# Kernel tuning notes

Hardware: AMD Instinct MI355X
Metric: run time of the kernel (lower is better)

## Reference

```python
import jax, jax.numpy as jnp
import numpy as np

B, L, D = 1, 1024, 128
EPS = 1e-5


def setup_inputs() -> dict:
    key = jax.random.key(0)
    ks = jax.random.split(key, 10)
    s = 1.0 / np.sqrt(D)
    return {
        "x": jax.random.normal(ks[0], (B, L, D), dtype=jnp.float32),
        "mask": jax.random.randint(ks[1], (B, L, L), 0, 2, dtype=jnp.int32),
        # JCrossOutProduct.l : Linear(D, D)
        "Wl": jax.random.uniform(ks[2], (D, D), jnp.float32, -s, s),
        "bl": jax.random.uniform(ks[3], (D,), jnp.float32, -s, s),
        # JCrossOutProduct.lo : Linear(D, D)
        "Wlo": jax.random.uniform(ks[4], (D, D), jnp.float32, -s, s),
        "blo": jax.random.uniform(ks[5], (D,), jnp.float32, -s, s),
        # JResCOPAttn.l : Linear(D, D)
        "Wl2": jax.random.uniform(ks[6], (D, D), jnp.float32, -s, s),
        "bl2": jax.random.uniform(ks[7], (D,), jnp.float32, -s, s),
        # LayerNorm(D)
        "gamma": jnp.ones((D,), jnp.float32),
        "beta": jnp.zeros((D,), jnp.float32),
    }


def reference(x, mask, Wl, bl, Wlo, blo, Wl2, bl2, gamma, beta):
    # a = self.cop.l(x) : [B, L, D]
    a = x @ Wl.T + bl
    # outer product kept per-channel: [B, L, L, D]
    outer = jnp.einsum('blc,bmc->blmc', a, a)
    # self.cop.lo over last dim: [B, L, L, D]
    tm = outer @ Wlo.T + blo
    # masked_fill(mask.unsqueeze(-1) == 0, 0.0)
    tm = tm * (mask[..., None] != 0).astype(tm.dtype)
    # tx = self.l(x)
    tx = x @ Wl2.T + bl2
    # per-channel attention-like contraction: out[b,c,d] = sum_a tm[b,c,a,d] * tx[b,a,d]
    y = x + jnp.einsum('bcad,bad->bcd', tm, tx)
    # shadow (eval): Dropout=identity, activator 'none'=identity, LayerNorm(D)
    mu = jnp.mean(y, axis=-1, keepdims=True)
    var = jnp.mean(jnp.square(y - mu), axis=-1, keepdims=True)
    return (y - mu) * jax.lax.rsqrt(var + EPS) * gamma + beta
```

## Files before the change

kernel.cpp:

```cpp
#include <hip/hip_runtime.h>
#include <hip/hip_fp16.h>


typedef _Float16 f16x8 __attribute__((ext_vector_type(8)));
typedef float    f32x4 __attribute__((ext_vector_type(4)));

#define LL   1024
#define DD   128
#define EPSV 1e-5f

__global__ __launch_bounds__(256) void prep_kernel(
    const float* __restrict__ x,  const float* __restrict__ Wl,
    const float* __restrict__ bl, const float* __restrict__ Wlo,
    const float* __restrict__ Wl2,const float* __restrict__ bl2,
    _Float16* __restrict__ a_h, float* __restrict__ tx_out,
    _Float16* __restrict__ wh)
{
    __shared__ float xs[16*128];
    __shared__ float wsh[64*129];
    const int t  = threadIdx.x;
    const int bx = blockIdx.x;
    const int by = blockIdx.y;
    const int l0 = by*16;

    #pragma unroll
    for (int i = 0; i < 8; ++i) { int f = i*256 + t; xs[f] = x[l0*DD + f]; }
    const float* Wsrc = ((bx < 2) ? Wl : Wl2) + (bx & 1)*64*DD;
    #pragma unroll
    for (int i = 0; i < 32; ++i) {
        int f = i*256 + t; int r = f >> 7, k = f & 127;
        wsh[r*129 + k] = Wsrc[f];
    }
    __syncthreads();

    const int col  = t & 63;
    const int lsub = t >> 6;
    const float4* X4 = (const float4*)xs;
    float acc0 = 0.f, acc1 = 0.f, acc2 = 0.f, acc3 = 0.f;
    #pragma unroll
    for (int k4 = 0; k4 < 32; ++k4) {
        const float* wp = wsh + col*129 + k4*4;
        float4 wv = {wp[0], wp[1], wp[2], wp[3]};
        float4 x0 = X4[(lsub*4+0)*32 + k4];
        float4 x1 = X4[(lsub*4+1)*32 + k4];
        float4 x2 = X4[(lsub*4+2)*32 + k4];
        float4 x3 = X4[(lsub*4+3)*32 + k4];
        acc0 += wv.x*x0.x + wv.y*x0.y + wv.z*x0.z + wv.w*x0.w;
        acc1 += wv.x*x1.x + wv.y*x1.y + wv.z*x1.z + wv.w*x1.w;
        acc2 += wv.x*x2.x + wv.y*x2.y + wv.z*x2.z + wv.w*x2.w;
        acc3 += wv.x*x3.x + wv.y*x3.y + wv.z*x3.z + wv.w*x3.w;
    }
    const int colg = (bx & 1)*64 + col;
    const float bv = ((bx < 2) ? bl : bl2)[colg];
    if (bx < 2) {
        a_h[(l0+lsub*4+0)*DD + colg] = (_Float16)(acc0 + bv);
        a_h[(l0+lsub*4+1)*DD + colg] = (_Float16)(acc1 + bv);
        a_h[(l0+lsub*4+2)*DD + colg] = (_Float16)(acc2 + bv);
        a_h[(l0+lsub*4+3)*DD + colg] = (_Float16)(acc3 + bv);
    } else {
        tx_out[(l0+lsub*4+0)*DD + colg] = acc0 + bv;
        tx_out[(l0+lsub*4+1)*DD + colg] = acc1 + bv;
        tx_out[(l0+lsub*4+2)*DD + colg] = acc2 + bv;
        tx_out[(l0+lsub*4+3)*DD + colg] = acc3 + bv;
    }

    const int gid = (by*4 + bx)*256 + t;
    if (gid < DD*DD) wh[gid] = (_Float16)Wlo[gid];
}

__global__ __launch_bounds__(256, 2) void heavy_kernel(
    const _Float16* __restrict__ a_h, const float* __restrict__ tx,
    const _Float16* __restrict__ wh,  const int* __restrict__ mask,
    const float* __restrict__ blo,    float* __restrict__ part)
{
    __shared__ __align__(16) _Float16 ash[64*DD];
    __shared__ __align__(16) float    txsh[64*DD];
    __shared__ float                  wmsh[32*64];
    const int t     = threadIdx.x;
    const int lane  = t & 63, w = t >> 6;
    const int chunk = blockIdx.x;
    const int ltile = blockIdx.y;
    const int l0 = ltile*32, m0 = chunk*64;

    {
        const float4* s4 = (const float4*)(a_h + m0*DD);
        float4* d4 = (float4*)ash;
        #pragma unroll
        for (int i = 0; i < 4; ++i) d4[i*256 + t] = s4[i*256 + t];
    }
    {
        const float4* s4 = (const float4*)(tx + m0*DD);
        float4* d4 = (float4*)txsh;
        #pragma unroll
        for (int i = 0; i < 8; ++i) d4[i*256 + t] = s4[i*256 + t];
    }
    {
        #pragma unroll
        for (int i = 0; i < 8; ++i) {
            int idx = i*256 + t;
            int row = idx >> 6, colm = idx & 63;
            wmsh[idx] = (mask[(l0 + row)*LL + m0 + colm] != 0) ? 1.f : 0.f;
        }
    }
    __syncthreads();

    const int grp = lane >> 4, ln = lane & 15;
    const int wl = w >> 1, wd = w & 1;
    const int lbase = l0 + wl*16;
    const int dbase = wd*64;

    f16x8 bh[4][4];
    #pragma unroll
    for (int nf = 0; nf < 4; ++nf)
        #pragma unroll
        for (int k = 0; k < 4; ++k)
            bh[nf][k] = *(const f16x8*)(wh + (dbase + nf*16 + ln)*DD + k*32 + grp*8);

    f16x8 al[4];
    #pragma unroll
    for (int k = 0; k < 4; ++k)
        al[k] = *(const f16x8*)(a_h + (lbase + ln)*DD + k*32 + grp*8);

    float blov[4];
    #pragma unroll
    for (int nf = 0; nf < 4; ++nf) blov[nf] = blo[dbase + nf*16 + ln];

    f32x4 y[4] = {{0,0,0,0},{0,0,0,0},{0,0,0,0},{0,0,0,0}};
    f32x4 S[4] = {{0,0,0,0},{0,0,0,0},{0,0,0,0},{0,0,0,0}};
    const int mrow0 = lbase + grp*4;
    const int wmbase = (wl*16 + grp*4)*64;

    #pragma unroll 2
    for (int ml = 0; ml < 64; ++ml) {
        float txd[4];
        #pragma unroll
        for (int nf = 0; nf < 4; ++nf) txd[nf] = txsh[ml*DD + dbase + nf*16 + ln];
        float wm[4];
        #pragma unroll
        for (int r = 0; r < 4; ++r) wm[r] = wmsh[wmbase + r*64 + ml];

        f16x8 ah[4];
        #pragma unroll
        for (int k = 0; k < 4; ++k)
            ah[k] = al[k] * *(const f16x8*)(ash + ml*DD + k*32 + grp*8);

        f32x4 c[4] = {{0,0,0,0},{0,0,0,0},{0,0,0,0},{0,0,0,0}};
        #pragma unroll
        for (int k = 0; k < 4; ++k) {
            c[0] = __builtin_amdgcn_mfma_f32_16x16x32_f16(ah[k], bh[0][k], c[0], 0,0,0);
            c[1] = __builtin_amdgcn_mfma_f32_16x16x32_f16(ah[k], bh[1][k], c[1], 0,0,0);
            c[2] = __builtin_amdgcn_mfma_f32_16x16x32_f16(ah[k], bh[2][k], c[2], 0,0,0);
            c[3] = __builtin_amdgcn_mfma_f32_16x16x32_f16(ah[k], bh[3][k], c[3], 0,0,0);
        }
        #pragma unroll
        for (int nf = 0; nf < 4; ++nf)
            #pragma unroll
            for (int r = 0; r < 4; ++r) {
                float s = wm[r]*txd[nf];
                y[nf][r] = fmaf(s, c[nf][r], y[nf][r]);
                S[nf][r] += s;
            }
    }

    float* dst = part + (size_t)chunk*(LL*DD);
    #pragma unroll
    for (int nf = 0; nf < 4; ++nf)
        #pragma unroll
        for (int r = 0; r < 4; ++r)
            dst[(mrow0 + r)*DD + dbase + nf*16 + ln] =
                fmaf(blov[nf], S[nf][r], y[nf][r]);
}

__global__ __launch_bounds__(128) void finish_kernel(
    const float* __restrict__ x, const float* __restrict__ part,
    const float* __restrict__ gamma, const float* __restrict__ beta,
    float* __restrict__ out)
{
    const int l = blockIdx.x, t = threadIdx.x;
    float v = x[l*DD + t];
    #pragma unroll
    for (int ch = 0; ch < 16; ++ch)
        v += part[((size_t)ch*LL + l)*DD + t];

    float s = v, s2 = v*v;
    #pragma unroll
    for (int o = 32; o > 0; o >>= 1) {
        s  += __shfl_xor(s, o);
        s2 += __shfl_xor(s2, o);
    }
    __shared__ float red[4];
    if ((t & 63) == 0) { red[(t>>6)*2+0] = s; red[(t>>6)*2+1] = s2; }
    __syncthreads();
    const float S  = red[0] + red[2];
    const float S2 = red[1] + red[3];
    const float mu  = S * (1.0f/128.0f);
    const float var = S2 * (1.0f/128.0f) - mu*mu;
    const float inv = rsqrtf(var + EPSV);
    out[l*DD + t] = (v - mu)*inv*gamma[t] + beta[t];
}

extern "C" void kernel_launch(void* const* d_in, const int* in_sizes, int n_in,
                              void* d_out, int out_size, void* d_ws, size_t ws_size,
                              hipStream_t stream)
{
    (void)in_sizes; (void)n_in; (void)out_size; (void)ws_size;
    const float* x     = (const float*)d_in[0];
    const int*   mask  = (const int*)  d_in[1];
    const float* Wl    = (const float*)d_in[2];
    const float* bl    = (const float*)d_in[3];
    const float* Wlo   = (const float*)d_in[4];
    const float* blo   = (const float*)d_in[5];
    const float* Wl2   = (const float*)d_in[6];
    const float* bl2   = (const float*)d_in[7];
    const float* gamma = (const float*)d_in[8];
    const float* beta  = (const float*)d_in[9];
    float* out = (float*)d_out;

    char* ws = (char*)d_ws;
    _Float16* a_h  = (_Float16*)(ws);
    float*    tx_b = (float*)   (ws + (256u<<10));
    _Float16* wh   = (_Float16*)(ws + (768u<<10));
    float*    part = (float*)   (ws + (1024u<<10));

    prep_kernel  <<<dim3(4,64),  256, 0, stream>>>(x, Wl, bl, Wlo, Wl2, bl2,
                                                   a_h, tx_b, wh);
    heavy_kernel <<<dim3(16,32), 256, 0, stream>>>(a_h, tx_b, wh, mask, blo, part);
    finish_kernel<<<1024, 128, 0, stream>>>(x, part, gamma, beta, out);
}
```

Measured before the change: 117.5 us.

## Shrink heavy kernel LDS with fp16 transposed tx and ballot mask bits, prefetch loop

The heavy kernel now stores tx in LDS as fp16 in a transposed, padded layout, and stores the mask as per-row 64-bit ballot bitmasks instead of a float array. This cuts shared memory use enough to raise the occupancy target from 2 to 3 blocks per CU. The bias is folded into the MFMA accumulator init, which removes the separate S accumulation. The inner loop is also software-pipelined with double-buffered register loads. Rounding tx to fp16 adds precision loss, and the tighter launch bound may cause register spills.

Result: slower. 133.9 us (+13.9%).

```diff
diff --git a/kernel.cpp b/kernel.cpp
--- a/kernel.cpp
+++ b/kernel.cpp
@@ -4,6 +4,8 @@
 
 typedef _Float16 f16x8 __attribute__((ext_vector_type(8)));
 typedef float    f32x4 __attribute__((ext_vector_type(4)));
+typedef unsigned int       u32;
+typedef unsigned long long u64;
 
 #define LL   1024
 #define DD   128
@@ -68,14 +70,14 @@
     if (gid < DD*DD) wh[gid] = (_Float16)Wlo[gid];
 }
 
-__global__ __launch_bounds__(256, 2) void heavy_kernel(
+__global__ __launch_bounds__(256, 3) void heavy_kernel(
     const _Float16* __restrict__ a_h, const float* __restrict__ tx,
     const _Float16* __restrict__ wh,  const int* __restrict__ mask,
     const float* __restrict__ blo,    float* __restrict__ part)
 {
     __shared__ __align__(16) _Float16 ash[64*DD];
-    __shared__ __align__(16) float    txsh[64*DD];
-    __shared__ float                  wmsh[32*64];
+    __shared__ __align__(4)  _Float16 txt[DD*66];
+    __shared__ u64 mbits[32];
     const int t     = threadIdx.x;
     const int lane  = t & 63, w = t >> 6;
     const int chunk = blockIdx.x;
@@ -89,17 +91,24 @@
         for (int i = 0; i < 4; ++i) d4[i*256 + t] = s4[i*256 + t];
     }
     {
-        const float4* s4 = (const float4*)(tx + m0*DD);
-        float4* d4 = (float4*)txsh;
-        #pragma unroll
-        for (int i = 0; i < 8; ++i) d4[i*256 + t] = s4[i*256 + t];
-    }
-    {
         #pragma unroll
         for (int i = 0; i < 8; ++i) {
             int idx = i*256 + t;
-            int row = idx >> 6, colm = idx & 63;
-            wmsh[idx] = (mask[(l0 + row)*LL + m0 + colm] != 0) ? 1.f : 0.f;
+            int m = idx >> 5, dg = idx & 31;
+            float4 v = *(const float4*)(tx + (m0+m)*DD + dg*4);
+            txt[(dg*4+0)*66 + m] = (_Float16)v.x;
+            txt[(dg*4+1)*66 + m] = (_Float16)v.y;
+            txt[(dg*4+2)*66 + m] = (_Float16)v.z;
+            txt[(dg*4+3)*66 + m] = (_Float16)v.w;
+        }
+    }
+    {
+        #pragma unroll
+        for (int i = 0; i < 8; ++i) {
+            int idx = i*256 + t;
+            int row = idx >> 6, mcol = idx & 63;
+            u64 b = __ballot(mask[(l0 + row)*LL + m0 + mcol] != 0);
+            if ((t & 63) == 0) mbits[row] = b;
         }
     }
     __syncthreads();
@@ -125,26 +134,21 @@
     #pragma unroll
     for (int nf = 0; nf < 4; ++nf) blov[nf] = blo[dbase + nf*16 + ln];
 
+    const int lrow0 = wl*16 + grp*4;
+    u64 wmb[4];
+    #pragma unroll
+    for (int r = 0; r < 4; ++r) wmb[r] = mbits[lrow0 + r];
+
     f32x4 y[4] = {{0,0,0,0},{0,0,0,0},{0,0,0,0},{0,0,0,0}};
-    f32x4 S[4] = {{0,0,0,0},{0,0,0,0},{0,0,0,0},{0,0,0,0}};
-    const int mrow0 = lbase + grp*4;
-    const int wmbase = (wl*16 + grp*4)*64;
-
-    #pragma unroll 2
-    for (int ml = 0; ml < 64; ++ml) {
-        float txd[4];
-        #pragma unroll
-        for (int nf = 0; nf < 4; ++nf) txd[nf] = txsh[ml*DD + dbase + nf*16 + ln];
-        float wm[4];
-        #pragma unroll
-        for (int r = 0; r < 4; ++r) wm[r] = wmsh[wmbase + r*64 + ml];
-
+
+    auto compute = [&](int m, const f16x8* am, const __half2* tp, bool hi) {
         f16x8 ah[4];
         #pragma unroll
-        for (int k = 0; k < 4; ++k)
-            ah[k] = al[k] * *(const f16x8*)(ash + ml*DD + k*32 + grp*8);
-
-        f32x4 c[4] = {{0,0,0,0},{0,0,0,0},{0,0,0,0},{0,0,0,0}};
+        for (int k = 0; k < 4; ++k) ah[k] = al[k] * am[k];
+        f32x4 c[4];
+        #pragma unroll
+        for (int nf = 0; nf < 4; ++nf)
+            c[nf] = f32x4{blov[nf], blov[nf], blov[nf], blov[nf]};
         #pragma unroll
         for (int k = 0; k < 4; ++k) {
             c[0] = __builtin_amdgcn_mfma_f32_16x16x32_f16(ah[k], bh[0][k], c[0], 0,0,0);
@@ -152,23 +156,62 @@
             c[2] = __builtin_amdgcn_mfma_f32_16x16x32_f16(ah[k], bh[2][k], c[2], 0,0,0);
             c[3] = __builtin_amdgcn_mfma_f32_16x16x32_f16(ah[k], bh[3][k], c[3], 0,0,0);
         }
+        float tv[4];
+        #pragma unroll
+        for (int nf = 0; nf < 4; ++nf) {
+            float2 f2 = __half22float2(tp[nf]);
+            tv[nf] = hi ? f2.y : f2.x;
+        }
+        #pragma unroll
+        for (int r = 0; r < 4; ++r) {
+            const bool on = ((wmb[r] >> m) & 1ull) != 0;
+            #pragma unroll
+            for (int nf = 0; nf < 4; ++nf) {
+                float s = on ? tv[nf] : 0.0f;
+                y[nf][r] = fmaf(s, c[nf][r], y[nf][r]);
+            }
+        }
+    };
+
+    f16x8 amA[4], amB[4];
+    __half2 tpA[4], tpB[4];
+    #pragma unroll
+    for (int k = 0; k < 4; ++k)
+        amA[k] = *(const f16x8*)(ash + 0*DD + k*32 + grp*8);
+    #pragma unroll
+    for (int nf = 0; nf < 4; ++nf)
+        tpA[nf] = *(const __half2*)(txt + (dbase + nf*16 + ln)*66 + 0);
+
+    for (int ms = 0; ms < 62; ms += 2) {
+        #pragma unroll
+        for (int k = 0; k < 4; ++k)
+            amB[k] = *(const f16x8*)(ash + (ms+1)*DD + k*32 + grp*8);
         #pragma unroll
         for (int nf = 0; nf < 4; ++nf)
-            #pragma unroll
-            for (int r = 0; r < 4; ++r) {
-                float s = wm[r]*txd[nf];
-                y[nf][r] = fmaf(s, c[nf][r], y[nf][r]);
-                S[nf][r] += s;
-            }
+            tpB[nf] = *(const __half2*)(txt + (dbase + nf*16 + ln)*66 + ms + 2);
+        compute(ms, amA, tpA, false);
+        #pragma unroll
+        for (int k = 0; k < 4; ++k)
+            amA[k] = *(const f16x8*)(ash + (ms+2)*DD + k*32 + grp*8);
+        compute(ms+1, amB, tpA, true);
+        #pragma unroll
+        for (int nf = 0; nf < 4; ++nf) tpA[nf] = tpB[nf];
+    }
+    {
+        #pragma unroll
+        for (int k = 0; k < 4; ++k)
+            amB[k] = *(const f16x8*)(ash + 63*DD + k*32 + grp*8);
+        compute(62, amA, tpA, false);
+        compute(63, amB, tpA, true);
     }
 
     float* dst = part + (size_t)chunk*(LL*DD);
+    const int mrow0 = lbase + grp*4;
     #pragma unroll
     for (int nf = 0; nf < 4; ++nf)
         #pragma unroll
         for (int r = 0; r < 4; ++r)
-            dst[(mrow0 + r)*DD + dbase + nf*16 + ln] =
-                fmaf(blov[nf], S[nf][r], y[nf][r]);
+            dst[(mrow0 + r)*DD + dbase + nf*16 + ln] = y[nf][r];
 }
 
 __global__ __launch_bounds__(128) void finish_kernel(
```
